# Optimization experiments

Hardware: AMD Instinct MI355X
Metric: run time of the kernel (lower is better)

The kernel has to match this reference:

```python
import jax, jax.numpy as jnp
import numpy as np

NUM_GROUPS = 512
GROUP_SIZE = 32
GROUP_RADIUS = 0.2
K_ORIGINAL = 5 * GROUP_SIZE  # ball_query oversampling factor from the source


def setup_inputs() -> dict:
    key = jax.random.key(0)
    k1, k2 = jax.random.split(key)
    B, N, C = 8, 16384, 4
    points = jax.random.normal(k1, (B, N, C), dtype=jnp.float32)
    # valid lengths in [N//2, N) so the lengths-masking path is exercised
    lengths = (N // 2 + jax.random.randint(k2, (B,), 0, N // 2)).astype(jnp.int32)
    return {"points": points, "lengths": lengths}


def _sample_farthest_points(xyz, lengths, K):
    # xyz: (B,N,3) float, lengths: (B,) int -> centers (B,K,3)
    B, N, _ = xyz.shape
    n_idx = jnp.arange(N)

    def per_batch(pts, length):
        valid = n_idx < length

        def step(carry, _):
            mindist, cur = carry
            d = jnp.sum((pts - pts[cur]) ** 2, axis=-1)  # (N,)
            mindist = jnp.where(valid, jnp.minimum(mindist, d), -jnp.inf)
            nxt = jnp.argmax(mindist).astype(jnp.int32)
            return (mindist, nxt), cur

        mindist0 = jnp.where(valid, jnp.inf, -jnp.inf)
        # deterministic start at index 0 (source uses random_start_point=True)
        (_, _), sel = jax.lax.scan(step, (mindist0, jnp.int32(0)), None, length=K)
        return pts[sel]

    return jax.vmap(per_batch)(xyz, lengths)


def _ball_query(centers, xyz, lengths, K, radius):
    # returns first-K (by point index, matching pytorch3d ball_query) indices
    # within radius; -1 padding. centers (B,G,3), xyz (B,N,3) -> idx (B,G,K)
    B, G, _ = centers.shape
    N = xyz.shape[1]
    d2 = jnp.sum((centers[:, :, None, :] - xyz[:, None, :, :]) ** 2, axis=-1)  # (B,G,N)
    valid = (jnp.arange(N) < lengths[:, None])[:, None, :]  # (B,1,N)
    mask = (d2 < radius * radius) & valid
    # score N-n > 0 iff in ball; top_k picks smallest indices first (in order)
    score = jnp.where(mask, N - jnp.arange(N, dtype=jnp.int32), jnp.int32(-1))
    vals, _ = jax.lax.top_k(score, K)
    return jnp.where(vals > 0, N - vals, -1)  # (B,G,K)


def _select_topk_by_energy(points, idx, K_new):
    # points (B,N,C), idx (B,G,K_orig) with -1 invalid -> (B,G,K_new)
    B, G, _ = idx.shape
    N = points.shape[1]
    invalid = idx == -1
    idxc = jnp.maximum(idx, 0)
    energies = jnp.broadcast_to(points[:, None, :, 3], (B, G, N))
    e = jnp.take_along_axis(energies, idxc, axis=2)  # (B,G,K_orig)
    e = jnp.where(invalid, -jnp.inf, e)
    top_e, top_i = jax.lax.top_k(e, K_new)
    topk_idx = jnp.take_along_axis(idx, top_i, axis=2)
    return jnp.where(top_e == -jnp.inf, -1, topk_idx)


def _masked_gather(points, idx):
    # points (B,N,C), idx (B,G,K); -1 -> gathered value 0.0 (pytorch3d semantics)
    B, G, K = idx.shape
    C = points.shape[-1]
    valid = idx >= 0
    flat = jnp.maximum(idx, 0).reshape(B, G * K)
    g = jnp.take_along_axis(points, flat[:, :, None], axis=1).reshape(B, G, K, C)
    return jnp.where(valid[..., None], g, 0.0)


def _forward(points, lengths):
    xyz = points[:, :, :3]
    centers = _sample_farthest_points(xyz, lengths, NUM_GROUPS)  # (B,G,3)
    idx = _ball_query(centers, xyz, lengths, K_ORIGINAL, GROUP_RADIUS)
    idx = _select_topk_by_energy(points, idx, GROUP_SIZE)  # (B,G,K)
    # fill_empty_indices: replace -1 with first index of the group
    first = idx[:, :, :1]
    idx = jnp.where(idx == -1, first, idx)
    groups = _masked_gather(points, idx)  # (B,G,K,C)
    groups = jnp.concatenate(
        [groups[..., :3] - centers[:, :, None, :], groups[..., 3:]], axis=-1
    )
    groups = groups / GROUP_RADIUS
    return groups, centers


def reference(points, lengths):
    return _forward(points, lengths)
```

## Files before the change

kernel.cpp:

```cpp
#include <hip/hip_runtime.h>

constexpr int B_ = 8;
constexpr int N_ = 16384;
constexpr int NG = 512;
constexpr int GS = 32;
constexpr int KORIG = 160;
constexpr int TPB = 512;
constexpr int PPT = 32;
#define R2 0.04f
#define RADIUS 0.2f

typedef __attribute__((ext_vector_type(2))) float f32x2;

__device__ __forceinline__ unsigned f32_ord(float f) {
  unsigned u = __float_as_uint(f);
  return (u & 0x80000000u) ? ~u : (u | 0x80000000u);
}

__device__ __forceinline__ f32x2 pk_add(f32x2 a, f32x2 b) {
  f32x2 d;
  asm("v_pk_add_f32 %0, %1, %2" : "=v"(d) : "v"(a), "v"(b));
  return d;
}
__device__ __forceinline__ f32x2 pk_mul(f32x2 a, f32x2 b) {
  f32x2 d;
  asm("v_pk_mul_f32 %0, %1, %2" : "=v"(d) : "v"(a), "v"(b));
  return d;
}

template <int CTRL>
__device__ __forceinline__ float dpp_fmax(float v) {
  int o = __builtin_amdgcn_update_dpp(0, __float_as_int(v), CTRL, 0xF, 0xF, true);
  return fmaxf(v, __int_as_float(o));
}
__device__ __forceinline__ float wave_fmax(float v) {
  v = dpp_fmax<0xB1>(v);
  v = dpp_fmax<0x4E>(v);
  v = dpp_fmax<0x141>(v);
  v = dpp_fmax<0x140>(v);
  v = fmaxf(v, __int_as_float(__builtin_amdgcn_ds_swizzle(__float_as_int(v), 0x401F)));
  v = fmaxf(v, __shfl_xor(v, 32, 64));
  return v;
}
__device__ __forceinline__ float group8_fmax(float v) {
  v = dpp_fmax<0xB1>(v);
  v = dpp_fmax<0x4E>(v);
  v = dpp_fmax<0x141>(v);
  return v;
}

__global__ __attribute__((amdgpu_flat_work_group_size(512, 512),
                          amdgpu_waves_per_eu(2, 2)))
void fps_kernel(const float4* __restrict__ p4,
                const int* __restrict__ lengths,
                float* __restrict__ centers) {
#pragma clang fp contract(off)
  const int b = blockIdx.x;
  const int t = threadIdx.x;
  const int lane = t & 63;
  const int wid = t >> 6;
  const int len = lengths[b];
  const float4* bp = p4 + (size_t)b * N_;
  const float INF = __builtin_inff();

  __shared__ float pubf[2][8];
  __shared__ int pubi[2][8];

  f32x2 x2[16], y2[16], z2[16], m2[16];
#pragma unroll
  for (int p = 0; p < 16; ++p) {
    const int i0 = t * PPT + 2 * p;
    float4 a = bp[i0];
    float4 c = bp[i0 + 1];
    x2[p] = (f32x2){a.x, c.x};
    y2[p] = (f32x2){a.y, c.y};
    z2[p] = (f32x2){a.z, c.z};
    m2[p].x = (i0 < len) ? INF : -INF;
    m2[p].y = (i0 + 1 < len) ? INF : -INF;
  }

  float4 c0 = bp[0];
  float cx = c0.x, cy = c0.y, cz = c0.z;
  if (t == 0) {
    size_t o = (size_t)b * NG * 3;
    centers[o] = cx; centers[o + 1] = cy; centers[o + 2] = cz;
  }

  for (int k = 0; k < NG - 1; ++k) {
    const f32x2 mcx = {-cx, -cx};
    const f32x2 mcy = {-cy, -cy};
    const f32x2 mcz = {-cz, -cz};
#pragma unroll
    for (int p = 0; p < 16; ++p) {
      f32x2 xx = pk_add(x2[p], mcx);
      f32x2 yy = pk_add(y2[p], mcy);
      f32x2 zz = pk_add(z2[p], mcz);
      f32x2 xs = pk_mul(xx, xx);
      f32x2 ys = pk_mul(yy, yy);
      f32x2 s1 = pk_add(xs, ys);
      f32x2 zs = pk_mul(zz, zz);
      f32x2 d2 = pk_add(s1, zs);
      m2[p].x = fminf(m2[p].x, d2.x);
      m2[p].y = fminf(m2[p].y, d2.y);
    }
    float pm[16];
#pragma unroll
    for (int i = 0; i < 16; ++i) pm[i] = fmaxf(m2[i].x, m2[i].y);
    float b8[8];
#pragma unroll
    for (int i = 0; i < 8; ++i) b8[i] = fmaxf(pm[2 * i], pm[2 * i + 1]);
    float b4[4];
#pragma unroll
    for (int i = 0; i < 4; ++i) b4[i] = fmaxf(b8[2 * i], b8[2 * i + 1]);
    float b2[2] = {fmaxf(b4[0], b4[1]), fmaxf(b4[2], b4[3])};
    const float sm = fmaxf(b2[0], b2[1]);

    const bool i1 = (b2[0] != sm);
    const float aL4 = i1 ? b4[2] : b4[0];
    const bool i2 = (aL4 != sm);
    const float aL8 = i1 ? (i2 ? b8[6] : b8[4]) : (i2 ? b8[2] : b8[0]);
    const bool i3 = (aL8 != sm);
    const float pmL = i1 ? (i2 ? (i3 ? pm[14] : pm[12]) : (i3 ? pm[10] : pm[8]))
                         : (i2 ? (i3 ? pm[6] : pm[4]) : (i3 ? pm[2] : pm[0]));
    const bool i4 = (pmL != sm);
    const int jp = ((int)i1 << 3) | ((int)i2 << 2) | ((int)i3 << 1) | (int)i4;
    const float mlo =
        i1 ? (i2 ? (i3 ? (i4 ? m2[15].x : m2[14].x) : (i4 ? m2[13].x : m2[12].x))
                 : (i3 ? (i4 ? m2[11].x : m2[10].x) : (i4 ? m2[9].x : m2[8].x)))
           : (i2 ? (i3 ? (i4 ? m2[7].x : m2[6].x) : (i4 ? m2[5].x : m2[4].x))
                 : (i3 ? (i4 ? m2[3].x : m2[2].x) : (i4 ? m2[1].x : m2[0].x)));
    const bool blo = (mlo != sm);
    const int gidx = t * PPT + jp * 2 + (int)blo;

    const float wmax = wave_fmax(sm);
    const unsigned long long att = __ballot(sm == wmax);
    const int wl = __ffsll(att) - 1;
    if (lane == wl) {
      pubf[k & 1][wid] = wmax;
      pubi[k & 1][wid] = gidx;
    }
    __syncthreads();

    const float pw = pubf[k & 1][lane & 7];
    const int pi = pubi[k & 1][lane & 7];
    const float kmax = group8_fmax(pw);
    const unsigned long long bal = __ballot(pw == kmax);
    const int grp = lane & 56;
    const int src = grp + (__ffsll((bal >> grp) & 0xFFull) - 1);
    const int gsel = __shfl(pi, src, 64);
    const int snxt = __builtin_amdgcn_readfirstlane(gsel);
    const float4 c = bp[snxt];
    cx = c.x; cy = c.y; cz = c.z;

    if (t == 0) {
      size_t o = ((size_t)b * NG + (k + 1)) * 3;
      centers[o] = cx; centers[o + 1] = cy; centers[o + 2] = cz;
    }
  }
}

__global__ __launch_bounds__(64) void group_kernel(const float4* __restrict__ p4,
                                                   const int* __restrict__ lengths,
                                                   const float* __restrict__ centers,
                                                   float4* __restrict__ outg) {
#pragma clang fp contract(off)
  const int gid = blockIdx.x;
  const int b = gid >> 9;
  const int lane = threadIdx.x;
  const int len = lengths[b];
  const float4* bp = p4 + (size_t)b * N_;
  const float cx = centers[(size_t)gid * 3 + 0];
  const float cy = centers[(size_t)gid * 3 + 1];
  const float cz = centers[(size_t)gid * 3 + 2];

  __shared__ int cand[KORIG];
  int M = 0;
  for (int cb = 0; cb < N_ && M < KORIG; cb += 256) {
#pragma unroll
    for (int q = 0; q < 4; ++q) {
      const int i = cb + q * 64 + lane;
      float4 p = bp[i];
      float dx = p.x - cx;
      float dy = p.y - cy;
      float dz = p.z - cz;
      float d2 = dx * dx + dy * dy + dz * dz;
      const bool pred = (i < len) && (d2 < R2);
      unsigned long long mb = __ballot(pred);
      if (pred) {
        int pos = M + (int)__popcll(mb & ((1ull << lane) - 1ull));
        if (pos < KORIG) cand[pos] = i;
      }
      M += (int)__popcll(mb);
    }
  }
  if (M > KORIG) M = KORIG;
  __syncthreads();

  const unsigned long long SENT = ~0ull;
  unsigned long long key0 = SENT, key1 = SENT, key2 = SENT;
  {
    int c0 = lane, c1 = lane + 64, c2 = lane + 128;
    if (c0 < M) { int i = cand[c0]; key0 = ((unsigned long long)(~f32_ord(bp[i].w)) << 32) | (unsigned)i; }
    if (c1 < M) { int i = cand[c1]; key1 = ((unsigned long long)(~f32_ord(bp[i].w)) << 32) | (unsigned)i; }
    if (c2 < M) { int i = cand[c2]; key2 = ((unsigned long long)(~f32_ord(bp[i].w)) << 32) | (unsigned)i; }
  }

  int mysel = -1;
  for (int j = 0; j < GS; ++j) {
    unsigned long long kmin = key0 < key1 ? key0 : key1;
    if (key2 < kmin) kmin = key2;
#pragma unroll
    for (int off = 32; off > 0; off >>= 1) {
      unsigned long long o = __shfl_xor(kmin, off, 64);
      if (o < kmin) kmin = o;
    }
    if (kmin == SENT) break;
    if (lane == j) mysel = (int)(unsigned)kmin;
    if (key0 == kmin) key0 = SENT;
    if (key1 == kmin) key1 = SENT;
    if (key2 == kmin) key2 = SENT;
  }

  const int first = __shfl(mysel, 0, 64);
  if (lane < GS) {
    int idx = (mysel < 0) ? first : mysel;
    float4 o;
    if (idx >= 0) {
      float4 p = bp[idx];
      o.x = (p.x - cx) / RADIUS;
      o.y = (p.y - cy) / RADIUS;
      o.z = (p.z - cz) / RADIUS;
      o.w = p.w / RADIUS;
    } else {
      o.x = (0.0f - cx) / RADIUS;
      o.y = (0.0f - cy) / RADIUS;
      o.z = (0.0f - cz) / RADIUS;
      o.w = 0.0f;
    }
    outg[(size_t)gid * GS + lane] = o;
  }
}

extern "C" void kernel_launch(void* const* d_in, const int* in_sizes, int n_in,
                              void* d_out, int out_size, void* d_ws, size_t ws_size,
                              hipStream_t stream) {
  const float4* pts = (const float4*)d_in[0];
  const int* lengths = (const int*)d_in[1];
  float* out = (float*)d_out;
  float* centers = out + (size_t)B_ * NG * GS * 4;
  float4* groups = (float4*)out;

  fps_kernel<<<B_, TPB, 0, stream>>>(pts, lengths, centers);
  group_kernel<<<B_ * NG, 64, 0, stream>>>(pts, lengths, centers, groups);
}
```

Before: 891.5 us.

## Replace per-iteration FPS block barrier with tagged atomic spin-wait publication

In the farthest-point-sampling loop, each wave's max distance and index are packed into one 64-bit LDS word together with the iteration number. Consumers spin on acquire loads until all 8 wave slots carry the current tag, so the `__syncthreads` barrier is no longer needed. The cross-wave argmax then becomes an unsigned-integer DPP reduction over lanes 0-7. This aims to cut barrier latency on the serial 511-step critical path, at the cost of busy-wait polling that competes for LDS bandwidth and issue slots.

After: 922.0 us. +3.4%, slower.

```diff
diff --git a/kernel.cpp b/kernel.cpp
--- a/kernel.cpp
+++ b/kernel.cpp
@@ -40,12 +40,6 @@
   v = dpp_fmax<0x140>(v);
   v = fmaxf(v, __int_as_float(__builtin_amdgcn_ds_swizzle(__float_as_int(v), 0x401F)));
   v = fmaxf(v, __shfl_xor(v, 32, 64));
-  return v;
-}
-__device__ __forceinline__ float group8_fmax(float v) {
-  v = dpp_fmax<0xB1>(v);
-  v = dpp_fmax<0x4E>(v);
-  v = dpp_fmax<0x141>(v);
   return v;
 }
 
@@ -63,8 +57,7 @@
   const float4* bp = p4 + (size_t)b * N_;
   const float INF = __builtin_inff();
 
-  __shared__ float pubf[2][8];
-  __shared__ int pubi[2][8];
+  __shared__ unsigned long long pub[2][8];
 
   f32x2 x2[16], y2[16], z2[16], m2[16];
 #pragma unroll
@@ -78,6 +71,8 @@
     m2[p].x = (i0 < len) ? INF : -INF;
     m2[p].y = (i0 + 1 < len) ? INF : -INF;
   }
+  if (t < 16) ((unsigned long long*)pub)[t] = ~0ull;
+  __syncthreads();
 
   float4 c0 = bp[0];
   float cx = c0.x, cy = c0.y, cz = c0.z;
@@ -135,19 +130,36 @@
     const float wmax = wave_fmax(sm);
     const unsigned long long att = __ballot(sm == wmax);
     const int wl = __ffsll(att) - 1;
+
     if (lane == wl) {
-      pubf[k & 1][wid] = wmax;
-      pubi[k & 1][wid] = gidx;
-    }
-    __syncthreads();
-
-    const float pw = pubf[k & 1][lane & 7];
-    const int pi = pubi[k & 1][lane & 7];
-    const float kmax = group8_fmax(pw);
-    const unsigned long long bal = __ballot(pw == kmax);
+      unsigned long long val = ((unsigned long long)f32_ord(wmax) << 32) |
+                               (unsigned)((k << 14) | gidx);
+      __hip_atomic_store(&pub[k & 1][wid], val, __ATOMIC_RELEASE,
+                         __HIP_MEMORY_SCOPE_WORKGROUP);
+    }
+    unsigned long long pv = 0;
+    const bool po = lane < 8;
+    for (;;) {
+      if (po) pv = __hip_atomic_load(&pub[k & 1][lane], __ATOMIC_ACQUIRE,
+                                     __HIP_MEMORY_SCOPE_WORKGROUP);
+      const bool ok = !po || (((unsigned)pv >> 14) == (unsigned)k);
+      if (__all(ok)) break;
+    }
+    const unsigned o0 = po ? (unsigned)(pv >> 32) : 0u;
+    unsigned km = o0;
+    {
+      int q;
+      q = __builtin_amdgcn_update_dpp(0, (int)km, 0xB1, 0xF, 0xF, true);
+      km = km > (unsigned)q ? km : (unsigned)q;
+      q = __builtin_amdgcn_update_dpp(0, (int)km, 0x4E, 0xF, 0xF, true);
+      km = km > (unsigned)q ? km : (unsigned)q;
+      q = __builtin_amdgcn_update_dpp(0, (int)km, 0x141, 0xF, 0xF, true);
+      km = km > (unsigned)q ? km : (unsigned)q;
+    }
+    const unsigned long long bal = __ballot(po && (o0 == km));
     const int grp = lane & 56;
     const int src = grp + (__ffsll((bal >> grp) & 0xFFull) - 1);
-    const int gsel = __shfl(pi, src, 64);
+    const int gsel = __shfl((int)((unsigned)pv & 0x3FFFu), src, 64);
     const int snxt = __builtin_amdgcn_readfirstlane(gsel);
     const float4 c = bp[snxt];
     cx = c.x; cy = c.y; cz = c.z;
```
